# Kernel tuning notes

Measured on AMD Instinct MI355X. Metric: run time of the kernel, lower is better.

## Reference

```python
import jax, jax.numpy as jnp
import numpy as np

NUM_HEADS = 8
D_CONV = 4
NORMALIZER = 16.0
LN_EPS = 1e-5


def setup_inputs() -> dict:
    key = jax.random.key(0)
    ks = jax.random.split(key, 9)
    B, L, E = 4, 2048, 1024
    dk = E // 2
    return {
        "x": jax.random.normal(ks[0], (B, L, E), jnp.float32),
        "conv_w": jax.random.normal(ks[1], (E, D_CONV), jnp.float32) * 0.3,
        "wq": jax.random.normal(ks[2], (E, dk), jnp.float32) * 0.02,
        "wkg": jax.random.normal(ks[3], (E, dk), jnp.float32) * 0.02,
        "wv": jax.random.normal(ks[4], (E, E), jnp.float32) * 0.02,
        "wg": jax.random.normal(ks[5], (E, E), jnp.float32) * 0.02,
        "bg": jax.random.normal(ks[6], (E,), jnp.float32) * 0.02,
        "wout": jax.random.normal(ks[7], (E, E), jnp.float32) * 0.02,
        "aug_balance": jax.random.normal(ks[8], (dk,), jnp.float32) * 0.1,
    }


def _causal_dwconv_silu(x, w):
    # x: [B, L, E]; w: [E, W] depthwise kernel. Causal: left-pad W-1 zeros.
    xt = jnp.transpose(x, (0, 2, 1))  # [B, E, L]
    y = jax.lax.conv_general_dilated(
        xt, w[:, None, :], window_strides=(1,), padding=[(w.shape[1] - 1, 0)],
        feature_group_count=x.shape[-1], dimension_numbers=("NCH", "OIH", "NCH"))
    return jnp.transpose(jax.nn.silu(y), (0, 2, 1))  # [B, L, E]


def _gla(q, k, v, gk, scale):
    # Gated linear attention recurrence (fused_chunk_gla math):
    #   S_t = S_{t-1} * exp(gk_t)[:, None] + k_t (outer) v_t
    #   o_t = (scale * q_t) @ S_t
    # q, k, gk: [B,H,L,Dk]; v: [B,H,L,Dv]
    B, H, L, Dk = q.shape
    Dv = v.shape[-1]

    def step(S, inp):
        qt, kt, vt, gt = inp  # [B,H,Dk], [B,H,Dk], [B,H,Dv], [B,H,Dk]
        S = S * jnp.exp(gt)[..., None] + kt[..., None] * vt[..., None, :]
        ot = jnp.einsum("bhk,bhkv->bhv", qt * scale, S)
        return S, ot

    mv = lambda a: jnp.moveaxis(a, 2, 0)  # L to leading axis for scan
    S0 = jnp.zeros((B, H, Dk, Dv), q.dtype)
    _, o = jax.lax.scan(step, S0, (mv(q), mv(k), mv(v), mv(gk)))
    return jnp.moveaxis(o, 0, 2)  # [B,H,L,Dv]


def reference(x, conv_w, wq, wkg, wv, wg, bg, wout, aug_balance):
    B, L, E = x.shape
    H = NUM_HEADS
    xc = _causal_dwconv_silu(x, conv_w)
    q = xc @ wq            # [B,L,dk]
    kg = xc @ wkg          # [B,L,dk]
    v = xc @ wv            # [B,L,E]
    g = xc @ wg + bg       # [B,L,E]

    gk = jax.nn.log_sigmoid(kg) / NORMALIZER
    k = 1.0 - jnp.exp(gk)

    dkh = q.shape[-1] // H  # key_dim per head
    to_heads = lambda t: t.reshape(B, L, H, -1).transpose(0, 2, 1, 3)
    qh, kh, vh, gkh = to_heads(q), to_heads(k), to_heads(v), to_heads(gk)

    scale = dkh ** -0.5
    o = _gla(qh, kh, vh, gkh, scale)  # [B,H,L,head_dim]

    # Augmented term: aug_w[b,h,l] = sum_d q[b,h,l,d] * aug[h,d] * k[b,h,l,d]
    aug = aug_balance.reshape(H, dkh)
    aug_w = jnp.einsum("bhld,hd,bhld->bhl", qh, aug, kh)
    o = o + jax.nn.sigmoid(aug_w[..., None] * vh)

    # LayerNorm over head_dim, no affine
    mu = o.mean(-1, keepdims=True)
    var = o.var(-1, keepdims=True)
    o = (o - mu) * jax.lax.rsqrt(var + LN_EPS)

    o = o.transpose(0, 2, 1, 3).reshape(B, L, E)
    return (jax.nn.silu(g) * o) @ wout
```

## Files before the change

### kernel.cpp

```cpp
#include <hip/hip_runtime.h>
#include <stdint.h>

typedef unsigned short u16;
typedef unsigned int u32;
typedef __attribute__((ext_vector_type(4))) float f32x4;
typedef __attribute__((ext_vector_type(8))) short short8;
typedef __attribute__((ext_vector_type(8))) _Float16 f16x8;

#define H 8
#define LSEQ 2048
#define E 1024
#define DK 512
#define DVH 128
#define DKH 64
#define NCHUNK 32
#define MROWS 8192
#define LN_EPS 1e-5f

#define AS1 __attribute__((address_space(1)))
#define AS3 __attribute__((address_space(3)))

static __device__ __forceinline__ float bf2f(u16 u) {
    union { float f; u32 i; } v; v.i = ((u32)u) << 16; return v.f;
}
static __device__ __forceinline__ u16 f2bf(float f) {
    union { float f; u32 i; } v; v.f = f;
    u32 r = v.i + 0x7FFFu + ((v.i >> 16) & 1u);
    return (u16)(r >> 16);
}

__global__ __launch_bounds__(256) void k_conv(const float* __restrict__ x,
                                              const float* __restrict__ cw,
                                              u16* __restrict__ xc) {
    const int l0 = blockIdx.x * 64;
    const int c  = blockIdx.y * 256 + threadIdx.x;
    const int b  = blockIdx.z;
    const f32x4 w = *(const f32x4*)(cw + c * 4);
    const float* base = x + (size_t)b * LSEQ * E + c;
    u16* ob = xc + (size_t)b * LSEQ * E + c;
    float x3 = (l0 >= 3) ? base[(size_t)(l0 - 3) * E] : 0.f;
    float x2 = (l0 >= 2) ? base[(size_t)(l0 - 2) * E] : 0.f;
    float x1 = (l0 >= 1) ? base[(size_t)(l0 - 1) * E] : 0.f;
#pragma unroll 8
    for (int r = 0; r < 64; r++) {
        const float x0 = base[(size_t)(l0 + r) * E];
        float a = x3 * w[0];
        a = fmaf(x2, w[1], a);
        a = fmaf(x1, w[2], a);
        a = fmaf(x0, w[3], a);
        const float s = a / (1.f + __expf(-a));
        ob[(size_t)(l0 + r) * E] = f2bf(s);
        x3 = x2; x2 = x1; x1 = x0;
    }
}

__global__ __launch_bounds__(256) void k_transpose_all(const float* __restrict__ wq,
                                                       const float* __restrict__ wkg,
                                                       const float* __restrict__ wv,
                                                       const float* __restrict__ wg,
                                                       const float* __restrict__ wout,
                                                       u16* __restrict__ wcat,
                                                       u16* __restrict__ woutT) {
    __shared__ float tile[32][33];
    const int z = blockIdx.z;
    const float* src; u16* dst; int Ncols;
    if (z == 0)      { src = wq;   dst = wcat;                        Ncols = 512; }
    else if (z == 1) { src = wkg;  dst = wcat + (size_t)512 * 1024;   Ncols = 512; }
    else if (z == 2) { src = wv;   dst = wcat + (size_t)1024 * 1024;  Ncols = 1024; }
    else if (z == 3) { src = wg;   dst = wcat + (size_t)2048 * 1024;  Ncols = 1024; }
    else             { src = wout; dst = woutT;                       Ncols = 1024; }
    const int n0 = blockIdx.x * 32, k0 = blockIdx.y * 32;
    if (n0 >= Ncols) return;
    const int K = 1024;
    const int tx = threadIdx.x & 31, ty = threadIdx.x >> 5;
#pragma unroll
    for (int p = 0; p < 4; p++) {
        const int r = p * 8 + ty;
        tile[r][tx] = src[(size_t)(k0 + r) * Ncols + n0 + tx];
    }
    __syncthreads();
#pragma unroll
    for (int p = 0; p < 4; p++) {
        const int rn = p * 8 + ty;
        dst[(size_t)(n0 + rn) * K + k0 + tx] = f2bf(tile[tx][rn]);
    }
}

__global__ __launch_bounds__(512, 1) void k_gemm0(const u16* __restrict__ A,
                                                  const u16* __restrict__ Bt,
                                                  u16* __restrict__ oQ, u16* __restrict__ oKG,
                                                  u16* __restrict__ oV, u16* __restrict__ oSG,
                                                  const float* __restrict__ bg) {
    const int K = 1024;
    __shared__ __align__(16) u16 smem[4][16384];
    const int tid = threadIdx.x;
    const int lane = tid & 63, wv = tid >> 6;
    const int wm = wv >> 2, wn = wv & 3;

    const int id = blockIdx.x;
    const int local = id >> 3;
    const int bx = ((id & 7) << 3) | (local & 7);
    const int by = local >> 3;

    const size_t rowBase = (size_t)bx * 128;
    const size_t colBase = (size_t)by * 384;

    const int rowIn = lane >> 2;
    const int uIn = lane & 3;

    auto stageA = [&](int hh) {
        u16* slotA = &smem[hh & 3][0];
        const u16* g = A + rowBase * K + hh * 32;
        const int row = wv * 16 + rowIn;
        const int sg = uIn ^ ((row >> 1) & 3);
        __builtin_amdgcn_global_load_lds(
            (const AS1 void*)(g + (size_t)row * K + sg * 8),
            (AS3 void*)(slotA + wv * 512), 16, 0, 0);
    };
    auto stageB = [&](int hh) {
        u16* slotB = &smem[hh & 3][4096];
        const u16* g = Bt + colBase * K + hh * 32;
#pragma unroll
        for (int i = 0; i < 3; i++) {
            const int row = i * 128 + wv * 16 + rowIn;
            const int sg = uIn ^ ((row >> 1) & 3);
            __builtin_amdgcn_global_load_lds(
                (const AS1 void*)(g + (size_t)row * K + sg * 8),
                (AS3 void*)(slotB + i * 4096 + wv * 512), 16, 0, 0);
        }
    };

    f32x4 acc[4][6];
#pragma unroll
    for (int m = 0; m < 4; m++)
#pragma unroll
        for (int n = 0; n < 6; n++) acc[m][n] = (f32x4){0.f, 0.f, 0.f, 0.f};

    const int rsub = lane & 15;
    const int cgl = lane >> 4;

    stageA(0); stageB(0);
    stageA(1); stageB(1);
    stageA(2); stageB(2);

    const int NT2 = K >> 5;
    for (int h = 0; h < NT2; h++) {
        const int rem = NT2 - 1 - h;
        if (rem >= 2)      asm volatile("s_waitcnt vmcnt(8)" ::: "memory");
        else if (rem == 1) asm volatile("s_waitcnt vmcnt(4)" ::: "memory");
        else               asm volatile("s_waitcnt vmcnt(0)" ::: "memory");
        asm volatile("s_barrier" ::: "memory");
        const u16* As = &smem[h & 3][0];
        const u16* Bs = As + 4096;
        short8 af[4], bfr[6];
#pragma unroll
        for (int mi = 0; mi < 4; mi++) {
            const int row = wm * 64 + mi * 16 + rsub;
            const int g = cgl ^ ((row >> 1) & 3);
            af[mi] = *(const short8*)(As + row * 32 + g * 8);
        }
#pragma unroll
        for (int ni = 0; ni < 6; ni++) {
            const int row = wn * 96 + ni * 16 + rsub;
            const int g = cgl ^ ((row >> 1) & 3);
            bfr[ni] = *(const short8*)(Bs + row * 32 + g * 8);
        }
        if (h + 3 < NT2) { stageA(h + 3); stageB(h + 3); }
        __builtin_amdgcn_s_setprio(1);
#pragma unroll
        for (int mi = 0; mi < 4; mi++)
#pragma unroll
            for (int ni = 0; ni < 6; ni++)
                acc[mi][ni] = __builtin_amdgcn_mfma_f32_16x16x32_bf16(af[mi], bfr[ni], acc[mi][ni], 0, 0, 0);
        __builtin_amdgcn_s_setprio(0);
    }

    const int r0 = (lane >> 4) * 4;
    u16* lds = &smem[0][0];
    __syncthreads();
#pragma unroll
    for (int ni = 0; ni < 6; ni++) {
        const int colg = (int)colBase + wn * 96 + ni * 16 + rsub;
        const bool isSG = (colg >= 2048);
        const float bgv = isSG ? bg[colg - 2048] : 0.f;
#pragma unroll
        for (int mi = 0; mi < 4; mi++) {
            const int lcol = wn * 96 + ni * 16 + rsub;
#pragma unroll
            for (int r = 0; r < 4; r++) {
                const int lrow = wm * 64 + mi * 16 + r0 + r;
                float val = acc[mi][ni][r];
                if (isSG) { const float y = val + bgv; val = y / (1.f + __expf(-y)); }
                lds[lrow * 384 + lcol] = f2bf(val);
            }
        }
    }
    __syncthreads();
    if (lane < 48) {
        const int col = (int)colBase + lane * 8;
        u16* seg; int stride; int c0;
        if (col < 512)       { seg = oQ;  stride = 512;  c0 = col; }
        else if (col < 1024) { seg = oKG; stride = 512;  c0 = col - 512; }
        else if (col < 2048) { seg = oV;  stride = 1024; c0 = col - 1024; }
        else                 { seg = oSG; stride = 1024; c0 = col - 2048; }
#pragma unroll
        for (int rr = 0; rr < 16; rr++) {
            const int lrow = wv * 16 + rr;
            const uint4 vv = *(const uint4*)(lds + lrow * 384 + lane * 8);
            *(uint4*)(seg + (rowBase + lrow) * (size_t)stride + c0) = vv;
        }
    }
}

__global__ __launch_bounds__(512, 1) void k_gemm1(const u16* __restrict__ A,
                                                  const u16* __restrict__ Bt,
                                                  float* __restrict__ oF) {
    const int K = 1024, N = 1024;
    __shared__ __align__(16) u16 smem[4][12288];
    const int tid = threadIdx.x;
    const int lane = tid & 63, wv = tid >> 6;
    const int wm = wv >> 1, wn = wv & 1;

    const int id = blockIdx.y * gridDim.x + blockIdx.x;
    const int bx = ((id & 7) << 2) | ((id >> 3) & 3);
    const int by = id >> 5;

    const size_t rowBase = (size_t)bx * 256;
    const size_t colBase = (size_t)by * 128;

    auto stageA = [&](int hh) {
        u16* slotA = &smem[hh & 3][0];
        const u16* g = A + rowBase * K + hh * 32;
#pragma unroll
        for (int i = 0; i < 2; i++) {
            const int r = i * 128 + wv * 16 + (lane >> 2);
            const int sg = (lane & 3) ^ ((r >> 1) & 3);
            __builtin_amdgcn_global_load_lds(
                (const AS1 void*)(g + (size_t)r * K + sg * 8),
                (AS3 void*)(slotA + i * 4096 + wv * 512), 16, 0, 0);
        }
    };
    auto stageB = [&](int hh) {
        u16* slotB = &smem[hh & 3][8192];
        const u16* g = Bt + colBase * K + hh * 32;
        const int r = wv * 16 + (lane >> 2);
        const int sg = (lane & 3) ^ ((r >> 1) & 3);
        __builtin_amdgcn_global_load_lds(
            (const AS1 void*)(g + (size_t)r * K + sg * 8),
            (AS3 void*)(slotB + wv * 512), 16, 0, 0);
    };

    f32x4 acc[4][4];
#pragma unroll
    for (int m = 0; m < 4; m++)
#pragma unroll
        for (int n = 0; n < 4; n++) acc[m][n] = (f32x4){0.f, 0.f, 0.f, 0.f};

    const int rsub = lane & 15;
    const int cgl = lane >> 4;

    stageA(0); stageB(0);
    stageA(1); stageB(1);
    stageA(2); stageB(2);

    const int NT2 = K >> 5;
    for (int h = 0; h < NT2; h++) {
        const int rem = NT2 - 1 - h;
        if (rem >= 2)      asm volatile("s_waitcnt vmcnt(6)" ::: "memory");
        else if (rem == 1) asm volatile("s_waitcnt vmcnt(3)" ::: "memory");
        else               asm volatile("s_waitcnt vmcnt(0)" ::: "memory");
        asm volatile("s_barrier" ::: "memory");
        const u16* As = &smem[h & 3][0];
        const u16* Bs = As + 8192;
        short8 af[4], bfr[4];
#pragma unroll
        for (int mi = 0; mi < 4; mi++) {
            const int row = wm * 64 + mi * 16 + rsub;
            const int g = cgl ^ ((row >> 1) & 3);
            af[mi] = *(const short8*)(As + row * 32 + g * 8);
        }
#pragma unroll
        for (int ni = 0; ni < 4; ni++) {
            const int row = wn * 64 + ni * 16 + rsub;
            const int g = cgl ^ ((row >> 1) & 3);
            bfr[ni] = *(const short8*)(Bs + row * 32 + g * 8);
        }
        if (h + 3 < NT2) { stageA(h + 3); stageB(h + 3); }
        __builtin_amdgcn_s_setprio(1);
#pragma unroll
        for (int mi = 0; mi < 4; mi++)
#pragma unroll
            for (int ni = 0; ni < 4; ni++)
                acc[mi][ni] = __builtin_amdgcn_mfma_f32_16x16x32_bf16(af[mi], bfr[ni], acc[mi][ni], 0, 0, 0);
        __builtin_amdgcn_s_setprio(0);
    }

    const int r0 = (lane >> 4) * 4;
    float* lf = (float*)&smem[0][0];
#pragma unroll
    for (int p = 0; p < 2; p++) {
        __syncthreads();
        if ((wm >> 1) == p) {
            const int wml = wm & 1;
#pragma unroll
            for (int mi = 0; mi < 4; mi++)
#pragma unroll
                for (int ni = 0; ni < 4; ni++) {
                    const int lcol = wn * 64 + ni * 16 + rsub;
#pragma unroll
                    for (int r = 0; r < 4; r++) {
                        const int lrow = wml * 64 + mi * 16 + r0 + r;
                        lf[lrow * 132 + lcol] = acc[mi][ni][r];
                    }
                }
        }
        __syncthreads();
#pragma unroll
        for (int i = 0; i < 8; i++) {
            const int unit = i * 512 + tid;
            const int row = unit >> 5, u = unit & 31;
            const f32x4 vv = *(const f32x4*)(lf + row * 132 + u * 4);
            *(f32x4*)(oF + (rowBase + p * 128 + row) * (size_t)N + colBase + u * 4) = vv;
        }
    }
}

__global__ __launch_bounds__(256) void k_gla1(const u16* __restrict__ q,
                                              const u16* __restrict__ kg,
                                              const u16* __restrict__ v,
                                              const float* __restrict__ aug,
                                              u16* __restrict__ qt,
                                              u16* __restrict__ obuf,
                                              float* __restrict__ Sd,
                                              float* __restrict__ Dc,
                                              float* __restrict__ augw) {
    __shared__ __align__(16) float    s_f[64][68];
    __shared__ __align__(16) _Float16 s_q[64][72];
    __shared__ __align__(16) _Float16 s_k[64][72];
    __shared__ __align__(16) _Float16 s_kT[64][72];
    __shared__ __align__(16) _Float16 s_a[64][72];
    __shared__ __align__(16) _Float16 s_vT[128][72];
    const int c = blockIdx.x, bh = blockIdx.y;
    const int b = bh >> 3, h = bh & 7;
    const int tid = threadIdx.x;
    const size_t rowBase = (size_t)b * LSEQ + c * 64;
    const size_t sdBase = (size_t)bh * NCHUNK + c;

    const int tA = tid >> 2, g4 = tid & 3;
    uint4 qr0, qr1;
    {
        const int d0 = g4 * 16;
        const u16* kp = kg + (rowBase + tA) * DK + h * 64 + d0;
        const uint4 k0 = *(const uint4*)kp;
        const uint4 k1 = *(const uint4*)(kp + 8);
        const u16 kv[16] = {
            (u16)(k0.x & 0xffff), (u16)(k0.x >> 16), (u16)(k0.y & 0xffff), (u16)(k0.y >> 16),
            (u16)(k0.z & 0xffff), (u16)(k0.z >> 16), (u16)(k0.w & 0xffff), (u16)(k0.w >> 16),
            (u16)(k1.x & 0xffff), (u16)(k1.x >> 16), (u16)(k1.y & 0xffff), (u16)(k1.y >> 16),
            (u16)(k1.z & 0xffff), (u16)(k1.z >> 16), (u16)(k1.w & 0xffff), (u16)(k1.w >> 16) };
#pragma unroll
        for (int j = 0; j < 16; j++) {
            const float xk = bf2f(kv[j]);
            const float ls = fminf(xk, 0.f) - __logf(1.f + __expf(-fabsf(xk)));
            s_f[tA][d0 + j] = ls * (1.f / 16.f);
        }
        const u16* qp = q + (rowBase + tA) * DK + h * 64 + d0;
        qr0 = *(const uint4*)qp;
        qr1 = *(const uint4*)(qp + 8);

        const int dv0 = g4 * 32;
        const u16* vp = v + (rowBase + tA) * E + h * 128 + dv0;
#pragma unroll
        for (int j8 = 0; j8 < 32; j8 += 8) {
            const uint4 u = *(const uint4*)(vp + j8);
            s_vT[dv0 + j8 + 0][tA] = (_Float16)bf2f((u16)(u.x & 0xffff));
            s_vT[dv0 + j8 + 1][tA] = (_Float16)bf2f((u16)(u.x >> 16));
            s_vT[dv0 + j8 + 2][tA] = (_Float16)bf2f((u16)(u.y & 0xffff));
            s_vT[dv0 + j8 + 3][tA] = (_Float16)bf2f((u16)(u.y >> 16));
            s_vT[dv0 + j8 + 4][tA] = (_Float16)bf2f((u16)(u.z & 0xffff));
            s_vT[dv0 + j8 + 5][tA] = (_Float16)bf2f((u16)(u.z >> 16));
            s_vT[dv0 + j8 + 6][tA] = (_Float16)bf2f((u16)(u.w & 0xffff));
            s_vT[dv0 + j8 + 7][tA] = (_Float16)bf2f((u16)(u.w >> 16));
        }
    }
    __syncthreads();

    {
        const int d = tid >> 2, qseg = tid & 3;
        float part = 0.f;
#pragma unroll
        for (int j = 0; j < 16; j++) part += s_f[qseg * 16 + j][d];
        float incl = part;
        const float u1 = __shfl_up(incl, 1, 4); if (qseg >= 1) incl += u1;
        const float u2 = __shfl_up(incl, 2, 4); if (qseg >= 2) incl += u2;
        float run = incl - part;
#pragma unroll
        for (int j = 0; j < 16; j++) {
            const int t = qseg * 16 + j;
            const float g = s_f[t][d];
            run += g;
            const float kk = 1.f - __expf(g);
            const float ktil = kk * __expf(-run);
            s_k[t][d] = (_Float16)ktil;
            s_kT[d][t] = (_Float16)ktil;
            s_a[t][d] = (_Float16)kk;
            s_f[t][d] = run;
        }
    }
    __syncthreads();

    {
        const int t = tA, d0 = g4 * 16;
        const u16 qv16[16] = {
            (u16)(qr0.x & 0xffff), (u16)(qr0.x >> 16), (u16)(qr0.y & 0xffff), (u16)(qr0.y >> 16),
            (u16)(qr0.z & 0xffff), (u16)(qr0.z >> 16), (u16)(qr0.w & 0xffff), (u16)(qr0.w >> 16),
            (u16)(qr1.x & 0xffff), (u16)(qr1.x >> 16), (u16)(qr1.y & 0xffff), (u16)(qr1.y >> 16),
            (u16)(qr1.z & 0xffff), (u16)(qr1.z >> 16), (u16)(qr1.w & 0xffff), (u16)(qr1.w >> 16) };
        float qv[16];
        float augp = 0.f;
#pragma unroll
        for (int j = 0; j < 16; j++) {
            const int d = d0 + j;
            const float qraw = bf2f(qv16[j]);
            const float L = s_f[t][d];
            const float kk = (float)s_a[t][d];
            const float qtv = qraw * __expf(L) * 0.125f;
            s_q[t][d] = (_Float16)qtv;
            qv[j] = qtv;
            augp = fmaf(qraw * aug[h * 64 + d], kk, augp);
        }
        u16* qto = qt + (rowBase + t) * DK + h * 64 + d0;
#pragma unroll
        for (int j8 = 0; j8 < 16; j8 += 8) {
            uint4 u;
            u.x = (u32)f2bf(qv[j8 + 0]) | ((u32)f2bf(qv[j8 + 1]) << 16);
            u.y = (u32)f2bf(qv[j8 + 2]) | ((u32)f2bf(qv[j8 + 3]) << 16);
            u.z = (u32)f2bf(qv[j8 + 4]) | ((u32)f2bf(qv[j8 + 5]) << 16);
            u.w = (u32)f2bf(qv[j8 + 6]) | ((u32)f2bf(qv[j8 + 7]) << 16);
            *(uint4*)(qto + j8) = u;
        }
        augp += __shfl_xor(augp, 1);
        augp += __shfl_xor(augp, 2);
        if ((tid & 3) == 0) augw[(size_t)bh * LSEQ + c * 64 + t] = augp;
    }
    __syncthreads();

    const int wv = tid >> 6, lane = tid & 63;
    const int rsub = lane & 15, kq8 = (lane >> 4) * 8, r0 = (lane >> 4) * 4;
    {
#pragma unroll
        for (int si = 0; si < 4; si++) {
            if (si <= wv) {
                f32x4 acc = (f32x4){0.f, 0.f, 0.f, 0.f};
#pragma unroll
                for (int kk = 0; kk < 2; kk++) {
                    const f16x8 af = *(const f16x8*)&s_q[wv * 16 + rsub][kk * 32 + kq8];
                    const f16x8 bf = *(const f16x8*)&s_k[si * 16 + rsub][kk * 32 + kq8];
                    acc = __builtin_amdgcn_mfma_f32_16x16x32_f16(af, bf, acc, 0, 0, 0);
                }
                const int scol = si * 16 + rsub;
#pragma unroll
                for (int r = 0; r < 4; r++) {
                    const int trow = wv * 16 + r0 + r;
                    const float val = (scol <= trow) ? acc[r] : 0.f;
                    s_a[trow][scol] = (_Float16)val;
                }
            } else {
#pragma unroll
                for (int r = 0; r < 4; r++)
                    s_a[wv * 16 + r0 + r][si * 16 + rsub] = (_Float16)0.f;
            }
        }
    }
    __syncthreads();

    {
        f32x4 oacc[8];
#pragma unroll
        for (int n = 0; n < 8; n++) oacc[n] = (f32x4){0.f, 0.f, 0.f, 0.f};
        const f16x8 a0 = *(const f16x8*)&s_a[wv * 16 + rsub][kq8];
        const f16x8 a1 = *(const f16x8*)&s_a[wv * 16 + rsub][32 + kq8];
#pragma unroll
        for (int n = 0; n < 8; n++) {
            const f16x8 b0 = *(const f16x8*)&s_vT[n * 16 + rsub][kq8];
            const f16x8 b1 = *(const f16x8*)&s_vT[n * 16 + rsub][32 + kq8];
            oacc[n] = __builtin_amdgcn_mfma_f32_16x16x32_f16(a0, b0, oacc[n], 0, 0, 0);
            oacc[n] = __builtin_amdgcn_mfma_f32_16x16x32_f16(a1, b1, oacc[n], 0, 0, 0);
        }
        u16* ob = obuf + ((size_t)bh * LSEQ + c * 64) * DVH;
#pragma unroll
        for (int n = 0; n < 8; n++) {
            const int dv = n * 16 + rsub;
#pragma unroll
            for (int r = 0; r < 4; r++) {
                const int trow = wv * 16 + r0 + r;
                ob[(size_t)trow * DVH + dv] = f2bf(oacc[n][r]);
            }
        }
    }

    {
        f32x4 sacc[8];
#pragma unroll
        for (int n = 0; n < 8; n++) sacc[n] = (f32x4){0.f, 0.f, 0.f, 0.f};
        const f16x8 a0 = *(const f16x8*)&s_kT[wv * 16 + rsub][kq8];
        const f16x8 a1 = *(const f16x8*)&s_kT[wv * 16 + rsub][32 + kq8];
#pragma unroll
        for (int n = 0; n < 8; n++) {
            const f16x8 b0 = *(const f16x8*)&s_vT[n * 16 + rsub][kq8];
            const f16x8 b1 = *(const f16x8*)&s_vT[n * 16 + rsub][32 + kq8];
            sacc[n] = __builtin_amdgcn_mfma_f32_16x16x32_f16(a0, b0, sacc[n], 0, 0, 0);
            sacc[n] = __builtin_amdgcn_mfma_f32_16x16x32_f16(a1, b1, sacc[n], 0, 0, 0);
        }
        float dend[4];
#pragma unroll
        for (int r = 0; r < 4; r++) dend[r] = __expf(s_f[63][wv * 16 + r0 + r]);
#pragma unroll
        for (int n = 0; n < 8; n++) {
            const int dv = n * 16 + rsub;
#pragma unroll
            for (int r = 0; r < 4; r++) {
                const int d = wv * 16 + r0 + r;
                Sd[(sdBase * DKH + d) * DVH + dv] = sacc[n][r] * dend[r];
            }
        }
        if (rsub == 0) {
#pragma unroll
            for (int r = 0; r < 4; r++) {
                const int d = wv * 16 + r0 + r;
                Dc[sdBase * DKH + d] = dend[r];
            }
        }
    }
}

__global__ __launch_bounds__(256) void k_gla2(const float* __restrict__ Sd,
                                              u16* __restrict__ Ss,
                                              const float* __restrict__ Dc) {
    const int cid = blockIdx.x * 256 + threadIdx.x;
    const int bh = cid >> 13;
    const int e = cid & 8191;
    const int d = e >> 7;
    float run = 0.f;
    const size_t base = (size_t)bh * NCHUNK * 8192 + e;
    for (int c = 0; c < NCHUNK; c++) {
        const size_t idx = base + (size_t)c * 8192;
        const float dl = Sd[idx];
        Ss[idx] = f2bf(run);
        run = fmaf(Dc[((size_t)bh * NCHUNK + c) * DKH + d], run, dl);
    }
}

__global__ __launch_bounds__(256) void k_gla3(const u16* __restrict__ qt,
                                              const u16* __restrict__ v,
                                              const u16* __restrict__ sg,
                                              const u16* __restrict__ obuf,
                                              const u16* __restrict__ Ss,
                                              const float* __restrict__ augw,
                                              u16* __restrict__ a2) {
    __shared__ __align__(16) _Float16 s_ST[128][72];
    __shared__ __align__(16) _Float16 s_qr[64][72];
    __shared__ __align__(16) float    s_O2[64][132];
    const int c = blockIdx.x, bh = blockIdx.y;
    const int b = bh >> 3, h = bh & 7;
    const int tid = threadIdx.x;
    const size_t rowBase = (size_t)b * LSEQ + c * 64;
    {
        const int d = tid >> 2, dv0 = (tid & 3) * 32;
        const u16* sp = Ss + (((size_t)bh * NCHUNK + c) * DKH + d) * DVH + dv0;
#pragma unroll
        for (int j8 = 0; j8 < 32; j8 += 8) {
            const uint4 u = *(const uint4*)(sp + j8);
            s_ST[dv0 + j8 + 0][d] = (_Float16)bf2f((u16)(u.x & 0xffff));
            s_ST[dv0 + j8 + 1][d] = (_Float16)bf2f((u16)(u.x >> 16));
            s_ST[dv0 + j8 + 2][d] = (_Float16)bf2f((u16)(u.y & 0xffff));
            s_ST[dv0 + j8 + 3][d] = (_Float16)bf2f((u16)(u.y >> 16));
            s_ST[dv0 + j8 + 4][d] = (_Float16)bf2f((u16)(u.z & 0xffff));
            s_ST[dv0 + j8 + 5][d] = (_Float16)bf2f((u16)(u.z >> 16));
            s_ST[dv0 + j8 + 6][d] = (_Float16)bf2f((u16)(u.w & 0xffff));
            s_ST[dv0 + j8 + 7][d] = (_Float16)bf2f((u16)(u.w >> 16));
        }
    }
    {
        const int t = tid >> 2, d0 = (tid & 3) * 16;
        const u16* qp = qt + (rowBase + t) * DK + h * 64 + d0;
        const uint4 q0 = *(const uint4*)qp;
        const uint4 q1 = *(const uint4*)(qp + 8);
        const u16 qv[16] = {
            (u16)(q0.x & 0xffff), (u16)(q0.x >> 16), (u16)(q0.y & 0xffff), (u16)(q0.y >> 16),
            (u16)(q0.z & 0xffff), (u16)(q0.z >> 16), (u16)(q0.w & 0xffff), (u16)(q0.w >> 16),
            (u16)(q1.x & 0xffff), (u16)(q1.x >> 16), (u16)(q1.y & 0xffff), (u16)(q1.y >> 16),
            (u16)(q1.z & 0xffff), (u16)(q1.z >> 16), (u16)(q1.w & 0xffff), (u16)(q1.w >> 16) };
#pragma unroll
        for (int j = 0; j < 16; j++) s_qr[t][d0 + j] = (_Float16)bf2f(qv[j]);
    }
    __syncthreads();
    {
        const int wv = tid >> 6, lane = tid & 63;
        const int rsub = lane & 15, kq8 = (lane >> 4) * 8, r0 = (lane >> 4) * 4;
        const f16x8 a0 = *(const f16x8*)&s_qr[wv * 16 + rsub][kq8];
        const f16x8 a1 = *(const f16x8*)&s_qr[wv * 16 + rsub][32 + kq8];
#pragma unroll
        for (int n = 0; n < 8; n++) {
            f32x4 acc = (f32x4){0.f, 0.f, 0.f, 0.f};
            const f16x8 b0 = *(const f16x8*)&s_ST[n * 16 + rsub][kq8];
            const f16x8 b1 = *(const f16x8*)&s_ST[n * 16 + rsub][32 + kq8];
            acc = __builtin_amdgcn_mfma_f32_16x16x32_f16(a0, b0, acc, 0, 0, 0);
            acc = __builtin_amdgcn_mfma_f32_16x16x32_f16(a1, b1, acc, 0, 0, 0);
            const int dv = n * 16 + rsub;
#pragma unroll
            for (int r = 0; r < 4; r++) s_O2[wv * 16 + r0 + r][dv] = acc[r];
        }
    }
    __syncthreads();
    const int t = tid >> 2, dv0 = (tid & 3) * 32;
    float o[32];
    const u16* op = obuf + ((size_t)bh * LSEQ + c * 64 + t) * DVH + dv0;
#pragma unroll
    for (int j8 = 0; j8 < 32; j8 += 8) {
        const uint4 u = *(const uint4*)(op + j8);
        o[j8 + 0] = bf2f((u16)(u.x & 0xffff)); o[j8 + 1] = bf2f((u16)(u.x >> 16));
        o[j8 + 2] = bf2f((u16)(u.y & 0xffff)); o[j8 + 3] = bf2f((u16)(u.y >> 16));
        o[j8 + 4] = bf2f((u16)(u.z & 0xffff)); o[j8 + 5] = bf2f((u16)(u.z >> 16));
        o[j8 + 6] = bf2f((u16)(u.w & 0xffff)); o[j8 + 7] = bf2f((u16)(u.w >> 16));
    }
#pragma unroll
    for (int j = 0; j < 32; j += 4) {
        const f32x4 sv = *(const f32x4*)&s_O2[t][dv0 + j];
        o[j + 0] += sv[0]; o[j + 1] += sv[1]; o[j + 2] += sv[2]; o[j + 3] += sv[3];
    }
    const float aw = augw[(size_t)bh * LSEQ + c * 64 + t];
    const u16* vp = v + (rowBase + t) * E + h * 128 + dv0;
#pragma unroll
    for (int j8 = 0; j8 < 32; j8 += 8) {
        const uint4 u = *(const uint4*)(vp + j8);
        const float vv[8] = {
            bf2f((u16)(u.x & 0xffff)), bf2f((u16)(u.x >> 16)),
            bf2f((u16)(u.y & 0xffff)), bf2f((u16)(u.y >> 16)),
            bf2f((u16)(u.z & 0xffff)), bf2f((u16)(u.z >> 16)),
            bf2f((u16)(u.w & 0xffff)), bf2f((u16)(u.w >> 16)) };
#pragma unroll
        for (int j = 0; j < 8; j++)
            o[j8 + j] += 1.f / (1.f + __expf(-aw * vv[j]));
    }
    float sum = 0.f;
#pragma unroll
    for (int j = 0; j < 32; j++) sum += o[j];
    sum += __shfl_xor(sum, 1); sum += __shfl_xor(sum, 2);
    const float mu = sum * (1.f / 128.f);
    float sq = 0.f;
#pragma unroll
    for (int j = 0; j < 32; j++) { const float dlt = o[j] - mu; sq = fmaf(dlt, dlt, sq); }
    sq += __shfl_xor(sq, 1); sq += __shfl_xor(sq, 2);
    const float rs = rsqrtf(sq * (1.f / 128.f) + LN_EPS);
    const u16* sp2 = sg + (rowBase + t) * E + h * 128 + dv0;
    u16* ap = a2 + (rowBase + t) * E + h * 128 + dv0;
#pragma unroll
    for (int j8 = 0; j8 < 32; j8 += 8) {
        const uint4 us = *(const uint4*)(sp2 + j8);
        const float sv[8] = {
            bf2f((u16)(us.x & 0xffff)), bf2f((u16)(us.x >> 16)),
            bf2f((u16)(us.y & 0xffff)), bf2f((u16)(us.y >> 16)),
            bf2f((u16)(us.z & 0xffff)), bf2f((u16)(us.z >> 16)),
            bf2f((u16)(us.w & 0xffff)), bf2f((u16)(us.w >> 16)) };
        uint4 u;
        u.x = (u32)f2bf(sv[0] * ((o[j8 + 0] - mu) * rs)) | ((u32)f2bf(sv[1] * ((o[j8 + 1] - mu) * rs)) << 16);
        u.y = (u32)f2bf(sv[2] * ((o[j8 + 2] - mu) * rs)) | ((u32)f2bf(sv[3] * ((o[j8 + 3] - mu) * rs)) << 16);
        u.z = (u32)f2bf(sv[4] * ((o[j8 + 4] - mu) * rs)) | ((u32)f2bf(sv[5] * ((o[j8 + 5] - mu) * rs)) << 16);
        u.w = (u32)f2bf(sv[6] * ((o[j8 + 6] - mu) * rs)) | ((u32)f2bf(sv[7] * ((o[j8 + 7] - mu) * rs)) << 16);
        *(uint4*)(ap + j8) = u;
    }
}

extern "C" void kernel_launch(void* const* d_in, const int* in_sizes, int n_in,
                              void* d_out, int out_size, void* d_ws, size_t ws_size,
                              hipStream_t stream) {
    const float* x      = (const float*)d_in[0];
    const float* conv_w = (const float*)d_in[1];
    const float* wq     = (const float*)d_in[2];
    const float* wkg    = (const float*)d_in[3];
    const float* wv     = (const float*)d_in[4];
    const float* wg     = (const float*)d_in[5];
    const float* bg     = (const float*)d_in[6];
    const float* wout   = (const float*)d_in[7];
    const float* aug    = (const float*)d_in[8];

    char* ws = (char*)d_ws;
    size_t off = 0;
    auto alloc = [&](size_t bytes) -> char* {
        char* p = ws + off;
        off += (bytes + 255) & ~(size_t)255;
        return p;
    };
    u16* xc    = (u16*)alloc((size_t)MROWS * E * 2);
    u16* wcat  = (u16*)alloc((size_t)3072 * E * 2);
    u16* woutT = (u16*)alloc((size_t)E * E * 2);
    u16* qb    = (u16*)alloc((size_t)MROWS * DK * 2);
    u16* kgb   = (u16*)alloc((size_t)MROWS * DK * 2);
    u16* vb    = (u16*)alloc((size_t)MROWS * E * 2);
    u16* sgb   = (u16*)alloc((size_t)MROWS * E * 2);
    u16* qtb   = (u16*)alloc((size_t)MROWS * DK * 2);
    u16* obuf  = (u16*)alloc((size_t)32 * LSEQ * DVH * 2);
    u16* Ssb   = (u16*)alloc((size_t)32 * NCHUNK * DKH * DVH * 2);
    float* Dc  = (float*)alloc((size_t)32 * NCHUNK * DKH * 4);
    float* augw= (float*)alloc((size_t)32 * LSEQ * 4);
    u16* a2    = qb;
    float* Sd  = (float*)d_out;

    k_conv<<<dim3(LSEQ / 64, E / 256, 4), 256, 0, stream>>>(x, conv_w, xc);
    k_transpose_all<<<dim3(32, 32, 5), 256, 0, stream>>>(wq, wkg, wv, wg, wout, wcat, woutT);
    k_gemm0<<<512, 512, 0, stream>>>(xc, wcat, qb, kgb, vb, sgb, bg);
    k_gla1<<<dim3(NCHUNK, 32), 256, 0, stream>>>(qb, kgb, vb, aug, qtb, obuf, Sd, Dc, augw);
    k_gla2<<<1024, 256, 0, stream>>>(Sd, Ssb, Dc);
    k_gla3<<<dim3(NCHUNK, 32), 256, 0, stream>>>(qtb, vb, sgb, obuf, Ssb, augw, a2);
    k_gemm1<<<dim3(32, 8), 512, 0, stream>>>(a2, woutT, (float*)d_out);
}
```

Before: 162.6 us.

## Shrink gemm0 tiles to 128x192 with 256 threads and store chunk states as bf16

The fused QKV/gate GEMM moves from 512-thread blocks with 128x384 tiles and a 4-deep pipeline to 256-thread blocks with 128x192 tiles and a 3-slot pipeline. The grid grows to 1024 blocks and LDS use shrinks, which should give better occupancy and load balance. The epilogue store is rewritten so all threads write coalesced 64-column slabs. Separately, the per-chunk state deltas passed between gla1 and gla2 are stored as bf16 instead of fp32, halving that traffic at the cost of precision in the recurrence inputs.

After: 155.5 us, median of 2. 4.4% less time.

```diff
diff --git a/kernel.cpp b/kernel.cpp
--- a/kernel.cpp
+++ b/kernel.cpp
@@ -86,16 +86,16 @@
     }
 }
 
-__global__ __launch_bounds__(512, 1) void k_gemm0(const u16* __restrict__ A,
+__global__ __launch_bounds__(256, 1) void k_gemm0(const u16* __restrict__ A,
                                                   const u16* __restrict__ Bt,
                                                   u16* __restrict__ oQ, u16* __restrict__ oKG,
                                                   u16* __restrict__ oV, u16* __restrict__ oSG,
                                                   const float* __restrict__ bg) {
     const int K = 1024;
-    __shared__ __align__(16) u16 smem[4][16384];
+    __shared__ __align__(16) u16 smem[3][10240];
     const int tid = threadIdx.x;
     const int lane = tid & 63, wv = tid >> 6;
-    const int wm = wv >> 2, wn = wv & 3;
+    const int wm = wv >> 1, wn = wv & 1;
 
     const int id = blockIdx.x;
     const int local = id >> 3;
@@ -103,30 +103,30 @@
     const int by = local >> 3;
 
     const size_t rowBase = (size_t)bx * 128;
-    const size_t colBase = (size_t)by * 384;
-
-    const int rowIn = lane >> 2;
-    const int uIn = lane & 3;
-
-    auto stageA = [&](int hh) {
-        u16* slotA = &smem[hh & 3][0];
-        const u16* g = A + rowBase * K + hh * 32;
-        const int row = wv * 16 + rowIn;
-        const int sg = uIn ^ ((row >> 1) & 3);
-        __builtin_amdgcn_global_load_lds(
-            (const AS1 void*)(g + (size_t)row * K + sg * 8),
-            (AS3 void*)(slotA + wv * 512), 16, 0, 0);
-    };
-    auto stageB = [&](int hh) {
-        u16* slotB = &smem[hh & 3][4096];
-        const u16* g = Bt + colBase * K + hh * 32;
+    const size_t colBase = (size_t)by * 192;
+
+    auto stage = [&](int hh, int sl) {
+        u16* slotA = &smem[sl][0];
+        u16* slotB = &smem[sl][4096];
+        const u16* gA = A + rowBase * K + hh * 32;
+        const u16* gB = Bt + colBase * K + hh * 32;
+#pragma unroll
+        for (int i = 0; i < 2; i++) {
+            const int u = i * 256 + wv * 64 + lane;
+            const int row = u >> 2;
+            const int sg = (u & 3) ^ ((row >> 1) & 3);
+            __builtin_amdgcn_global_load_lds(
+                (const AS1 void*)(gA + (size_t)row * K + sg * 8),
+                (AS3 void*)(slotA + (i * 256 + wv * 64) * 8), 16, 0, 0);
+        }
 #pragma unroll
         for (int i = 0; i < 3; i++) {
-            const int row = i * 128 + wv * 16 + rowIn;
-            const int sg = uIn ^ ((row >> 1) & 3);
+            const int u = i * 256 + wv * 64 + lane;
+            const int row = u >> 2;
+            const int sg = (u & 3) ^ ((row >> 1) & 3);
             __builtin_amdgcn_global_load_lds(
-                (const AS1 void*)(g + (size_t)row * K + sg * 8),
-                (AS3 void*)(slotB + i * 4096 + wv * 512), 16, 0, 0);
+                (const AS1 void*)(gB + (size_t)row * K + sg * 8),
+                (AS3 void*)(slotB + (i * 256 + wv * 64) * 8), 16, 0, 0);
         }
     };
 
@@ -139,19 +139,16 @@
     const int rsub = lane & 15;
     const int cgl = lane >> 4;
 
-    stageA(0); stageB(0);
-    stageA(1); stageB(1);
-    stageA(2); stageB(2);
+    stage(0, 0); stage(1, 1);
 
     const int NT2 = K >> 5;
     for (int h = 0; h < NT2; h++) {
-        const int rem = NT2 - 1 - h;
-        if (rem >= 2)      asm volatile("s_waitcnt vmcnt(8)" ::: "memory");
-        else if (rem == 1) asm volatile("s_waitcnt vmcnt(4)" ::: "memory");
-        else               asm volatile("s_waitcnt vmcnt(0)" ::: "memory");
+        if (h + 1 < NT2) asm volatile("s_waitcnt vmcnt(5)" ::: "memory");
+        else             asm volatile("s_waitcnt vmcnt(0)" ::: "memory");
         asm volatile("s_barrier" ::: "memory");
-        const u16* As = &smem[h & 3][0];
-        const u16* Bs = As + 4096;
+        const int sl = h % 3;
+        const u16* As = &smem[sl][0];
+        const u16* Bs = &smem[sl][4096];
         short8 af[4], bfr[6];
 #pragma unroll
         for (int mi = 0; mi < 4; mi++) {
@@ -165,7 +162,7 @@
             const int g = cgl ^ ((row >> 1) & 3);
             bfr[ni] = *(const short8*)(Bs + row * 32 + g * 8);
         }
-        if (h + 3 < NT2) { stageA(h + 3); stageB(h + 3); }
+        if (h + 2 < NT2) stage(h + 2, (h + 2) % 3);
         __builtin_amdgcn_s_setprio(1);
 #pragma unroll
         for (int mi = 0; mi < 4; mi++)
@@ -183,31 +180,33 @@
         const int colg = (int)colBase + wn * 96 + ni * 16 + rsub;
         const bool isSG = (colg >= 2048);
         const float bgv = isSG ? bg[colg - 2048] : 0.f;
+        const int lcol = wn * 96 + ni * 16 + rsub;
 #pragma unroll
         for (int mi = 0; mi < 4; mi++) {
-            const int lcol = wn * 96 + ni * 16 + rsub;
 #pragma unroll
             for (int r = 0; r < 4; r++) {
                 const int lrow = wm * 64 + mi * 16 + r0 + r;
                 float val = acc[mi][ni][r];
                 if (isSG) { const float y = val + bgv; val = y / (1.f + __expf(-y)); }
-                lds[lrow * 384 + lcol] = f2bf(val);
+                lds[lrow * 192 + lcol] = f2bf(val);
             }
         }
     }
     __syncthreads();
-    if (lane < 48) {
-        const int col = (int)colBase + lane * 8;
+#pragma unroll
+    for (int sp = 0; sp < 3; sp++) {
+        const int gc = (int)colBase + sp * 64;
         u16* seg; int stride; int c0;
-        if (col < 512)       { seg = oQ;  stride = 512;  c0 = col; }
-        else if (col < 1024) { seg = oKG; stride = 512;  c0 = col - 512; }
-        else if (col < 2048) { seg = oV;  stride = 1024; c0 = col - 1024; }
-        else                 { seg = oSG; stride = 1024; c0 = col - 2048; }
-#pragma unroll
-        for (int rr = 0; rr < 16; rr++) {
-            const int lrow = wv * 16 + rr;
-            const uint4 vv = *(const uint4*)(lds + lrow * 384 + lane * 8);
-            *(uint4*)(seg + (rowBase + lrow) * (size_t)stride + c0) = vv;
+        if (gc < 512)       { seg = oQ;  stride = 512;  c0 = gc; }
+        else if (gc < 1024) { seg = oKG; stride = 512;  c0 = gc - 512; }
+        else if (gc < 2048) { seg = oV;  stride = 1024; c0 = gc - 1024; }
+        else                { seg = oSG; stride = 1024; c0 = gc - 2048; }
+#pragma unroll
+        for (int i = 0; i < 4; i++) {
+            const int unit = i * 256 + tid;
+            const int row = unit >> 3, uu = unit & 7;
+            const uint4 vv = *(const uint4*)(lds + row * 192 + sp * 64 + uu * 8);
+            *(uint4*)(seg + (rowBase + row) * (size_t)stride + c0 + uu * 8) = vv;
         }
     }
 }
@@ -331,7 +330,7 @@
                                               const float* __restrict__ aug,
                                               u16* __restrict__ qt,
                                               u16* __restrict__ obuf,
-                                              float* __restrict__ Sd,
+                                              u16* __restrict__ Sd,
                                               float* __restrict__ Dc,
                                               float* __restrict__ augw) {
     __shared__ __align__(16) float    s_f[64][68];
@@ -521,7 +520,7 @@
 #pragma unroll
             for (int r = 0; r < 4; r++) {
                 const int d = wv * 16 + r0 + r;
-                Sd[(sdBase * DKH + d) * DVH + dv] = sacc[n][r] * dend[r];
+                Sd[(sdBase * DKH + d) * DVH + dv] = f2bf(sacc[n][r] * dend[r]);
             }
         }
         if (rsub == 0) {
@@ -534,7 +533,7 @@
     }
 }
 
-__global__ __launch_bounds__(256) void k_gla2(const float* __restrict__ Sd,
+__global__ __launch_bounds__(256) void k_gla2(const u16* __restrict__ Sd,
                                               u16* __restrict__ Ss,
                                               const float* __restrict__ Dc) {
     const int cid = blockIdx.x * 256 + threadIdx.x;
@@ -545,7 +544,7 @@
     const size_t base = (size_t)bh * NCHUNK * 8192 + e;
     for (int c = 0; c < NCHUNK; c++) {
         const size_t idx = base + (size_t)c * 8192;
-        const float dl = Sd[idx];
+        const float dl = bf2f(Sd[idx]);
         Ss[idx] = f2bf(run);
         run = fmaf(Dc[((size_t)bh * NCHUNK + c) * DKH + d], run, dl);
     }
@@ -705,11 +704,11 @@
     float* Dc  = (float*)alloc((size_t)32 * NCHUNK * DKH * 4);
     float* augw= (float*)alloc((size_t)32 * LSEQ * 4);
     u16* a2    = qb;
-    float* Sd  = (float*)d_out;
+    u16* Sd    = (u16*)d_out;
 
     k_conv<<<dim3(LSEQ / 64, E / 256, 4), 256, 0, stream>>>(x, conv_w, xc);
     k_transpose_all<<<dim3(32, 32, 5), 256, 0, stream>>>(wq, wkg, wv, wg, wout, wcat, woutT);
-    k_gemm0<<<512, 512, 0, stream>>>(xc, wcat, qb, kgb, vb, sgb, bg);
+    k_gemm0<<<1024, 256, 0, stream>>>(xc, wcat, qb, kgb, vb, sgb, bg);
     k_gla1<<<dim3(NCHUNK, 32), 256, 0, stream>>>(qb, kgb, vb, aug, qtb, obuf, Sd, Dc, augw);
     k_gla2<<<1024, 256, 0, stream>>>(Sd, Ssb, Dc);
     k_gla3<<<dim3(NCHUNK, 32), 256, 0, stream>>>(qtb, vb, sgb, obuf, Ssb, augw, a2);
```
